# Performance work log

Hardware: AMD Instinct MI355X
Metric: run time of the kernel (lower is better)

## Reference

```python
import jax, jax.numpy as jnp
import numpy as np

B = 16; SEQ_LEN = 96; PRED_LEN = 96; N_VARS = 862; D_MODEL = 512; D_FF = 1024
N_HEADS = 8; E_LAYERS = 2; D_FREQ = 512; KF_LEN = 5000; ALPHA = 0.5; TOP_P = 0.5
FREQ_DIM = SEQ_LEN // 2 + 1            # rfft bins = 49
KEY_LEN = int(np.ceil(FREQ_DIM * ALPHA))  # 25 -> y_freq in_features = 50
KERNEL = 25; NOISE_EPS = 0.01; LN_EPS = 1e-5; REVIN_EPS = 1e-5


def setup_inputs() -> dict:
    ks = iter(jax.random.split(jax.random.key(0), 64))
    def g(*shape):
        return jax.random.normal(next(ks), shape, jnp.float32) * 0.02
    z = lambda *s: jnp.zeros(s, jnp.float32)
    o = lambda *s: jnp.ones(s, jnp.float32)
    inp = {}
    inp['x_enc'] = jax.random.normal(next(ks), (B, SEQ_LEN, N_VARS), jnp.float32)
    inp['gate_noise'] = jax.random.normal(next(ks), (N_VARS,), jnp.float32)
    inp['revin_w'] = o(N_VARS); inp['revin_b'] = z(N_VARS)
    inp['fc2_w'] = g(SEQ_LEN, D_MODEL); inp['fc2_b'] = z(D_MODEL)
    inp['fc3_w'] = g(D_MODEL, PRED_LEN); inp['fc3_b'] = z(PRED_LEN)
    inp['fc4_w'] = g(SEQ_LEN, D_MODEL); inp['fc4_b'] = z(D_MODEL)
    inp['fc5_w'] = g(D_MODEL, PRED_LEN); inp['fc5_b'] = z(PRED_LEN)
    inp['tc_w1'] = g(D_MODEL, D_MODEL // 2); inp['tc_w2'] = g(D_MODEL // 2, N_VARS)
    inp['tn_w1'] = g(D_MODEL, D_MODEL // 2); inp['tn_w2'] = g(D_MODEL // 2, N_VARS)
    inp['lt_w1'] = g(SEQ_LEN, D_MODEL); inp['lt_b1'] = z(D_MODEL)
    inp['lt_w2'] = g(D_MODEL, D_MODEL); inp['lt_b2'] = z(D_MODEL)
    inp['yf_w'] = g(2 * KEY_LEN, D_FREQ); inp['yf_b'] = z(D_FREQ)
    inp['ls_w1'] = g(D_FREQ, D_FREQ); inp['ls_b1'] = z(D_FREQ)
    inp['ls_w2'] = g(D_FREQ, D_FREQ); inp['ls_b2'] = z(D_FREQ)
    inp['fco_w'] = g(2 * D_MODEL, PRED_LEN); inp['fco_b'] = z(PRED_LEN)
    inp['freq_table'] = jax.random.normal(next(ks), (KF_LEN, N_VARS), jnp.float32)
    inp['enc_wq'] = g(E_LAYERS, D_MODEL, D_MODEL); inp['enc_bq'] = z(E_LAYERS, D_MODEL)
    inp['enc_wk'] = g(E_LAYERS, D_MODEL, D_MODEL); inp['enc_bk'] = z(E_LAYERS, D_MODEL)
    inp['enc_wv'] = g(E_LAYERS, D_MODEL, D_MODEL); inp['enc_bv'] = z(E_LAYERS, D_MODEL)
    inp['enc_wo'] = g(E_LAYERS, D_MODEL, D_MODEL); inp['enc_bo'] = z(E_LAYERS, D_MODEL)
    inp['enc_c1w'] = g(E_LAYERS, D_MODEL, D_FF); inp['enc_c1b'] = z(E_LAYERS, D_FF)
    inp['enc_c2w'] = g(E_LAYERS, D_FF, D_MODEL); inp['enc_c2b'] = z(E_LAYERS, D_MODEL)
    inp['enc_g1'] = o(E_LAYERS, D_MODEL); inp['enc_be1'] = z(E_LAYERS, D_MODEL)
    inp['enc_g2'] = o(E_LAYERS, D_MODEL); inp['enc_be2'] = z(E_LAYERS, D_MODEL)
    inp['norm_g'] = o(D_MODEL); inp['norm_b'] = z(D_MODEL)
    inp['batch_key_frequency'] = jax.random.randint(next(ks), (B,), 0, KF_LEN)
    return inp


def _lrelu(t):
    return jnp.where(t >= 0, t, 0.01 * t)


def _layernorm(x, g, b):
    m = jnp.mean(x, -1, keepdims=True)
    v = jnp.mean((x - m) ** 2, -1, keepdims=True)
    return (x - m) * jax.lax.rsqrt(v + LN_EPS) * g + b


def _decomp(x):
    # moving_avg(kernel=25, stride=1) with edge replication padding, via cumsum
    pad = (KERNEL - 1) // 2
    xp = jnp.concatenate([jnp.repeat(x[:, :1], pad, axis=1), x,
                          jnp.repeat(x[:, -1:], pad, axis=1)], axis=1)
    c = jnp.cumsum(xp, axis=1)
    c = jnp.concatenate([jnp.zeros_like(c[:, :1]), c], axis=1)
    mean = (c[:, KERNEL:] - c[:, :-KERNEL]) / KERNEL  # [B, L, N]
    return x - mean, mean


def _kf_gather(table, index, length):
    # data[(index[:,None] + arange(length)) % KF_LEN] -> [B, length, N]
    gi = (index[:, None] + jnp.arange(length)[None, :]) % KF_LEN
    return table[gi]


def _forward(x_enc, gate_noise, revin_w, revin_b, fc2_w, fc2_b, fc3_w, fc3_b,
             fc4_w, fc4_b, fc5_w, fc5_b, tc_w1, tc_w2, tn_w1, tn_w2,
             lt_w1, lt_b1, lt_w2, lt_b2, yf_w, yf_b, ls_w1, ls_b1, ls_w2, ls_b2,
             fco_w, fco_b, freq_table, enc_wq, enc_bq, enc_wk, enc_bk, enc_wv, enc_bv,
             enc_wo, enc_bo, enc_c1w, enc_c1b, enc_c2w, enc_c2b,
             enc_g1, enc_be1, enc_g2, enc_be2, norm_g, norm_b, batch_key_frequency):
    # RevIN norm (stats detached, as in RevIN)
    mean = jax.lax.stop_gradient(jnp.mean(x_enc, axis=1, keepdims=True))
    std = jax.lax.stop_gradient(jnp.sqrt(jnp.var(x_enc, axis=1, keepdims=True) + REVIN_EPS))
    x = (x_enc - mean) / std * revin_w + revin_b  # [B, L, N]

    # ---- Frequency encoder ----
    _, trend = _decomp(x)
    t = _lrelu(trend.transpose(0, 2, 1) @ lt_w1 + lt_b1) @ lt_w2 + lt_b2  # [B,N,D]
    xf = jnp.fft.rfft(x.transpose(0, 2, 1), axis=-1, norm='ortho')  # [B,N,FREQ_DIM]
    y_key = jnp.concatenate([xf.real[..., :KEY_LEN], xf.imag[..., :KEY_LEN]], axis=-1)
    y_key = y_key @ yf_w + yf_b  # [B,N,D_FREQ]
    y_key = y_key.transpose(0, 2, 1) - _kf_gather(freq_table, batch_key_frequency, D_FREQ)
    y = _lrelu(y_key.transpose(0, 2, 1) @ ls_w1 + ls_b1) @ ls_w2 + ls_b2  # [B,N,D_FREQ]
    y = y.transpose(0, 2, 1) + _kf_gather(freq_table, (batch_key_frequency + D_FREQ) % KF_LEN, D_FREQ)
    y = y.transpose(0, 2, 1)  # [B,N,D_FREQ], real part of frequency coeffs
    x_fre = jnp.fft.irfft(y.astype(jnp.complex64), n=SEQ_LEN, axis=-1, norm='ortho')  # [B,N,L]
    x_fre = x_fre @ fc4_w + fc4_b + t  # [B,N,D]
    x_fre_loss = x_fre @ fc5_w + fc5_b  # [B,N,pred]

    # ---- Time encoder ----
    xb = x.transpose(0, 2, 1) @ fc2_w + fc2_b  # [B,N,D]
    # noisy top-p gating mask
    xc = jax.nn.relu(xb @ tc_w1) @ tc_w2
    xn = jax.nn.relu(xb @ tn_w1) @ tn_w2
    # nn.Softplus(beta=-1): -log(1+exp(-x)) = -softplus(-x)
    xe = xc + gate_noise * (-jax.nn.softplus(-(xn + NOISE_EPS)))
    xmin = jnp.min(xe, axis=-1, keepdims=True)
    xmax = jnp.max(xe, axis=-1, keepdims=True)
    logits = (xe - xmin) / (xmax - xmin + 1e-6) + jnp.eye(N_VARS, dtype=xe.dtype)
    mask = (logits < TOP_P)[:, None]  # [B,1,N,N], True = masked out

    scale = 1.0 / np.sqrt(D_MODEL // N_HEADS)
    for l in range(E_LAYERS):
        q = (xb @ enc_wq[l] + enc_bq[l]).reshape(B, N_VARS, N_HEADS, -1)
        k = (xb @ enc_wk[l] + enc_bk[l]).reshape(B, N_VARS, N_HEADS, -1)
        v = (xb @ enc_wv[l] + enc_bv[l]).reshape(B, N_VARS, N_HEADS, -1)
        s = jnp.einsum('blhe,bshe->bhls', q, k)
        s = jnp.where(mask, -jnp.inf, s)
        a = jax.nn.softmax(scale * s, axis=-1)
        o = jnp.einsum('bhls,bshd->blhd', a, v).reshape(B, N_VARS, D_MODEL)
        xb = xb + (o @ enc_wo[l] + enc_bo[l])
        xb = _layernorm(xb, enc_g1[l], enc_be1[l])
        yff = jax.nn.gelu(xb @ enc_c1w[l] + enc_c1b[l], approximate=False) @ enc_c2w[l] + enc_c2b[l]
        xb = _layernorm(xb + yff, enc_g2[l], enc_be2[l])
    xb = _layernorm(xb, norm_g, norm_b)
    x_time_loss = xb @ fc3_w + fc3_b  # [B,N,pred]

    dec = (jnp.concatenate([xb, x_fre], axis=-1) @ fco_w + fco_b).transpose(0, 2, 1)  # [B,pred,N]

    def _denorm(z):
        return ((z - revin_b) / (revin_w + REVIN_EPS * REVIN_EPS)) * std + mean

    dec = _denorm(dec)
    x_time_loss = _denorm(x_time_loss.transpose(0, 2, 1))
    x_fre_loss = _denorm(x_fre_loss.transpose(0, 2, 1))
    return dec[:, -PRED_LEN:, :], x_time_loss, x_fre_loss


def reference(x_enc, gate_noise, revin_w, revin_b, fc2_w, fc2_b, fc3_w, fc3_b,
              fc4_w, fc4_b, fc5_w, fc5_b, tc_w1, tc_w2, tn_w1, tn_w2,
              lt_w1, lt_b1, lt_w2, lt_b2, yf_w, yf_b, ls_w1, ls_b1, ls_w2, ls_b2,
              fco_w, fco_b, freq_table, enc_wq, enc_bq, enc_wk, enc_bk, enc_wv, enc_bv,
              enc_wo, enc_bo, enc_c1w, enc_c1b, enc_c2w, enc_c2b,
              enc_g1, enc_be1, enc_g2, enc_be2, norm_g, norm_b, batch_key_frequency):
    return _forward(x_enc, gate_noise, revin_w, revin_b, fc2_w, fc2_b, fc3_w, fc3_b,
                    fc4_w, fc4_b, fc5_w, fc5_b, tc_w1, tc_w2, tn_w1, tn_w2,
                    lt_w1, lt_b1, lt_w2, lt_b2, yf_w, yf_b, ls_w1, ls_b1, ls_w2, ls_b2,
                    fco_w, fco_b, freq_table, enc_wq, enc_bq, enc_wk, enc_bk, enc_wv, enc_bv,
                    enc_wo, enc_bo, enc_c1w, enc_c1b, enc_c2w, enc_c2b,
                    enc_g1, enc_be1, enc_g2, enc_be2, norm_g, norm_b, batch_key_frequency)
```

## Files before the change

kernel.cpp:

```cpp
#include <hip/hip_runtime.h>
#include <hip/hip_bf16.h>
#include <math.h>

typedef __hip_bfloat16 bf16;
typedef unsigned long long u64;
using s8v = __attribute__((ext_vector_type(8))) short;
using f4v = __attribute__((ext_vector_type(4))) float;

#define B_   16
#define L_   96
#define NV   862
#define DM   512
#define NH   8
#define DH   64
#define KFL  5000
#define NBN  (B_*NV)
#define TS   72
#define NVP  896
#define QKVW 1536

__device__ __forceinline__ float tof(bf16 x)  { return __bfloat162float(x); }

__device__ __forceinline__ int sx(int r, int k) {
    return r * TS + (((k >> 3) ^ (r & 7)) << 3) + (k & 7);
}
__device__ __forceinline__ int sxc(int r, int c) {
    return r * TS + ((c ^ (r & 7)) << 3);
}

__global__ void detect_k(const unsigned short* __restrict__ rw, int* __restrict__ flag)
{
    if (threadIdx.x == 0 && blockIdx.x == 0)
        *flag = (rw[0] == 0 && rw[2] == 0 && rw[4] == 0) ? 1 : 0;
}

struct CB { const void* src[30]; bf16* dst[30]; int n[30]; int so[30]; };
__global__ __launch_bounds__(256)
void cvtb_k(CB cb, const int* __restrict__ flag)
{
    int t = blockIdx.y;
    int i = blockIdx.x * 256 + threadIdx.x;
    if (i >= cb.n[t]) return;
    int s = cb.so[t] + i;
    if (*flag) cb.dst[t][i] = __float2bfloat16(((const float*)cb.src[t])[s]);
    else       cb.dst[t][i] = ((const bf16*)cb.src[t])[s];
}

#define NWT 24
struct WD { const void* src; bf16* dst; int K, N; long srcOff; };
struct WTB { WD d[NWT]; };
__global__ __launch_bounds__(256)
void wtcb_k(WTB wb, const int* __restrict__ flag)
{
    __shared__ bf16 tile[32][33];
    WD dd = wb.d[blockIdx.z];
    int n0 = blockIdx.x * 32, k0 = blockIdx.y * 32;
    if (n0 >= dd.N || k0 >= dd.K) return;
    int tx = threadIdx.x & 31, ty = threadIdx.x >> 5;
    int f32 = *flag;
    #pragma unroll
    for (int r = 0; r < 4; r++) {
        int k = k0 + ty + r * 8, n = n0 + tx;
        bf16 v = __float2bfloat16(0.f);
        if (k < dd.K && n < dd.N)
            v = f32 ? __float2bfloat16(((const float*)dd.src)[dd.srcOff + (size_t)k * dd.N + n])
                    : ((const bf16*)dd.src)[dd.srcOff + (size_t)k * dd.N + n];
        tile[ty + r * 8][tx] = v;
    }
    __syncthreads();
    #pragma unroll
    for (int r = 0; r < 4; r++) {
        int n = n0 + ty + r * 8, k = k0 + tx;
        if (n < dd.N && k < dd.K) dd.dst[(size_t)n * dd.K + k] = tile[tx][ty + r * 8];
    }
}

__global__ __launch_bounds__(256)
void vt_k(const bf16* __restrict__ qkv, bf16* __restrict__ Vt)
{
    __shared__ bf16 t[32][33];
    int bh = blockIdx.z;
    int n0 = blockIdx.x * 32, d0 = blockIdx.y * 32;
    int b = bh >> 3, h = bh & 7;
    int tx = threadIdx.x & 31, ty = threadIdx.x >> 5;
    #pragma unroll
    for (int r = 0; r < 4; r++) {
        int n = n0 + ty + r * 8, d = d0 + tx;
        bf16 v = __float2bfloat16(0.f);
        if (n < NV) v = qkv[(size_t)(b * NV + n) * QKVW + 1024 + h * DH + d];
        t[ty + r * 8][tx] = v;
    }
    __syncthreads();
    #pragma unroll
    for (int r = 0; r < 4; r++) {
        int d = d0 + ty + r * 8, n = n0 + tx;
        Vt[((size_t)bh * DH + d) * NVP + n] = t[tx][ty + r * 8];
    }
}

__global__ __launch_bounds__(128)
void revin_k(const void* __restrict__ x_enc, const bf16* __restrict__ rw,
             const bf16* __restrict__ rb, bf16* __restrict__ xT,
             bf16* __restrict__ trend, float* __restrict__ meanA,
             float* __restrict__ stdA, const int* __restrict__ flag)
{
    int row = blockIdx.x;
    int b = row / NV, n = row - b * NV;
    int tid = threadIdx.x;
    int f32 = *flag;
    __shared__ float xr[96];
    __shared__ float part[2][2];
    __shared__ float mv[2];
    float v = 0.f;
    if (tid < 96) {
        size_t idx = ((size_t)b * L_ + tid) * NV + n;
        v = f32 ? ((const float*)x_enc)[idx] : tof(((const bf16*)x_enc)[idx]);
    }
    float s = v, sq = v * v;
    #pragma unroll
    for (int off = 32; off; off >>= 1) {
        s  += __shfl_xor(s,  off, 64);
        sq += __shfl_xor(sq, off, 64);
    }
    int wid = tid >> 6;
    if ((tid & 63) == 0) { part[wid][0] = s; part[wid][1] = sq; }
    __syncthreads();
    if (tid == 0) {
        float S = part[0][0] + part[1][0], Q = part[0][1] + part[1][1];
        float m = S / 96.f;
        float var = fmaxf(Q / 96.f - m * m, 0.f);
        float st = sqrtf(var + 1e-5f);
        mv[0] = m; mv[1] = st;
        meanA[row] = m; stdA[row] = st;
    }
    __syncthreads();
    float m = mv[0], st = mv[1];
    if (tid < 96) {
        float xv = (v - m) / st * tof(rw[n]) + tof(rb[n]);
        xr[tid] = xv;
        xT[(size_t)row * L_ + tid] = __float2bfloat16(xv);
    }
    __syncthreads();
    if (tid < 96) {
        float acc = 0.f;
        #pragma unroll
        for (int d = -12; d <= 12; d++) {
            int k = tid + d;
            k = k < 0 ? 0 : (k > 95 ? 95 : k);
            acc += xr[k];
        }
        trend[(size_t)row * L_ + tid] = __float2bfloat16(acc * (1.f / 25.f));
    }
}

__global__ void myf_k(const bf16* __restrict__ yf_w, bf16* __restrict__ MyfT)
{
    int idx = blockIdx.x * 256 + threadIdx.x;
    if (idx >= 96 * 512) return;
    int l = idx / 512, d = idx - l * 512;
    const float invs = 0.10206207261596575f;
    float acc = 0.f;
    for (int f = 0; f < 25; f++) {
        float ang = (float)(f * l) / 48.0f;
        acc += cospif(ang) * tof(yf_w[f * 512 + d]);
        acc -= sinpif(ang) * tof(yf_w[(25 + f) * 512 + d]);
    }
    MyfT[(size_t)d * 96 + l] = __float2bfloat16(acc * invs);
}

__global__ void ceff_k(const bf16* __restrict__ fc4_w, bf16* __restrict__ CeffT)
{
    int idx = blockIdx.x * 256 + threadIdx.x;
    if (idx >= 49 * 512) return;
    int f = idx / 512, d = idx - f * 512;
    const float invs = 0.10206207261596575f;
    float acc = 0.f;
    for (int l = 0; l < 96; l++) {
        float coef;
        if (f == 0)       coef = 1.f;
        else if (f == 48) coef = (l & 1) ? -1.f : 1.f;
        else              coef = 2.f * cospif((float)(f * l) / 48.f);
        acc += coef * tof(fc4_w[l * 512 + d]);
    }
    CeffT[(size_t)d * 49 + f] = __float2bfloat16(acc * invs);
}

__device__ __forceinline__ float epi(float v, int n, int m, int N, int act,
                                     const bf16* bias, const float* Res,
                                     const void* ft, const int* kf,
                                     const int* dflag)
{
    if (act >= 5) {
        v += tof(bias[n]);
        int b = m / NV, nv = m - b * NV;
        int gi = (act == 5) ? (kf[b] + n) % KFL : (kf[b] + 512 + n) % KFL;
        size_t gidx = (size_t)gi * NV + nv;
        float fv = (*dflag) ? ((const float*)ft)[gidx] : tof(((const bf16*)ft)[gidx]);
        return (act == 5) ? v - fv : v + fv;
    }
    if (act == 4) {
        float z = -(v + 0.01f);
        float sp = fmaxf(z, 0.f) + log1pf(expf(-fabsf(z)));
        return Res[(size_t)m * N + n] + tof(bias[n]) * (-sp);
    }
    if (bias) v += tof(bias[n]);
    if (Res)  v += Res[(size_t)m * N + n];
    if (act == 1)      v = fmaxf(v, 0.f);
    else if (act == 2) v = (v >= 0.f) ? v : 0.01f * v;
    else if (act == 3) v = 0.5f * v * (1.f + erff(v * 0.70710678118654752f));
    return v;
}

__global__ __launch_bounds__(256)
void gemm_mfma(const bf16* __restrict__ A, int lda,
               const bf16* __restrict__ Wt, int ldb,
               const bf16* __restrict__ bias, const float* Res,
               float* C32, bf16* C16, int M, int N, int K, int act,
               const void* ft, const int* kf, const int* dflag)
{
    __shared__ bf16 As[64 * TS];
    __shared__ bf16 Bs[64 * TS];
    int tid = threadIdx.x;
    int w = tid >> 6, lane = tid & 63;
    int lr = lane >> 4, lc = lane & 15;
    int row0 = blockIdx.y * 64, col0 = blockIdx.x * 64;
    int mq = (w >> 1) * 32, nq = (w & 1) * 32;
    f4v acc[2][2] = {};
    bool vecA = ((lda & 7) == 0) && ((K & 7) == 0);
    bool vecB = ((ldb & 7) == 0) && ((K & 7) == 0);
    const bf16 z16 = __float2bfloat16(0.f);
    for (int k0 = 0; k0 < K; k0 += 64) {
        if (vecA) {
            int r = tid >> 2, c0 = tid & 3;
            #pragma unroll
            for (int hh = 0; hh < 2; hh++) {
                int c = c0 + hh * 4;
                int gr = row0 + r, gk = k0 + c * 8;
                uint4 v = make_uint4(0, 0, 0, 0);
                if (gr < M && gk < K) v = *(const uint4*)(A + (size_t)gr * lda + gk);
                *(uint4*)&As[sxc(r, c)] = v;
            }
        } else {
            for (int i = tid; i < 4096; i += 256) {
                int r = i >> 6, k = i & 63;
                int gr = row0 + r, gk = k0 + k;
                As[sx(r, k)] = (gr < M && gk < K) ? A[(size_t)gr * lda + gk] : z16;
            }
        }
        if (vecB) {
            int r = tid >> 2, c0 = tid & 3;
            #pragma unroll
            for (int hh = 0; hh < 2; hh++) {
                int c = c0 + hh * 4;
                int gr = col0 + r, gk = k0 + c * 8;
                uint4 v = make_uint4(0, 0, 0, 0);
                if (gr < N && gk < K) v = *(const uint4*)(Wt + (size_t)gr * ldb + gk);
                *(uint4*)&Bs[sxc(r, c)] = v;
            }
        } else {
            for (int i = tid; i < 4096; i += 256) {
                int r = i >> 6, k = i & 63;
                int gr = col0 + r, gk = k0 + k;
                Bs[sx(r, k)] = (gr < N && gk < K) ? Wt[(size_t)gr * ldb + gk] : z16;
            }
        }
        __syncthreads();
        #pragma unroll
        for (int sub = 0; sub < 2; sub++) {
            int ck = sub * 4 + lr;
            s8v a0 = *(const s8v*)&As[sxc(mq + lc, ck)];
            s8v a1 = *(const s8v*)&As[sxc(mq + 16 + lc, ck)];
            s8v b0 = *(const s8v*)&Bs[sxc(nq + lc, ck)];
            s8v b1 = *(const s8v*)&Bs[sxc(nq + 16 + lc, ck)];
            acc[0][0] = __builtin_amdgcn_mfma_f32_16x16x32_bf16(a0, b0, acc[0][0], 0, 0, 0);
            acc[0][1] = __builtin_amdgcn_mfma_f32_16x16x32_bf16(a0, b1, acc[0][1], 0, 0, 0);
            acc[1][0] = __builtin_amdgcn_mfma_f32_16x16x32_bf16(a1, b0, acc[1][0], 0, 0, 0);
            acc[1][1] = __builtin_amdgcn_mfma_f32_16x16x32_bf16(a1, b1, acc[1][1], 0, 0, 0);
        }
        __syncthreads();
    }
    #pragma unroll
    for (int mt = 0; mt < 2; mt++)
    #pragma unroll
    for (int nt = 0; nt < 2; nt++) {
        #pragma unroll
        for (int r = 0; r < 4; r++) {
            int m = row0 + mq + mt * 16 + lr * 4 + r;
            int n = col0 + nq + nt * 16 + lc;
            if (m >= M || n >= N) continue;
            float v = epi(acc[mt][nt][r], n, m, N, act, bias, Res, ft, kf, dflag);
            if (C32) C32[(size_t)m * N + n] = v;
            if (C16) C16[(size_t)m * N + n] = __float2bfloat16(v);
        }
    }
}

__global__ __launch_bounds__(256)
void gemm128(const bf16* __restrict__ A, int lda,
             const bf16* __restrict__ Wt, int ldb,
             const bf16* __restrict__ bias, const float* Res,
             float* C32, bf16* C16, int M, int N, int K, int act)
{
    __shared__ bf16 As[128 * TS];
    __shared__ bf16 Bs[128 * TS];
    int tid = threadIdx.x;
    int w = tid >> 6, lane = tid & 63;
    int lr = lane >> 4, lc = lane & 15;
    int row0 = blockIdx.y * 128, col0 = blockIdx.x * 128;
    int mq = (w >> 1) * 64, nq = (w & 1) * 64;
    f4v acc[4][4] = {};
    for (int k0 = 0; k0 < K; k0 += 64) {
        #pragma unroll
        for (int i = 0; i < 4; i++) {
            int e = tid + i * 256;
            int r = e >> 3, c = e & 7;
            int gr = row0 + r, gk = k0 + c * 8;
            uint4 v = make_uint4(0, 0, 0, 0);
            if (gr < M && gk < K) v = *(const uint4*)(A + (size_t)gr * lda + gk);
            *(uint4*)&As[sxc(r, c)] = v;
        }
        #pragma unroll
        for (int i = 0; i < 4; i++) {
            int e = tid + i * 256;
            int r = e >> 3, c = e & 7;
            int gr = col0 + r, gk = k0 + c * 8;
            uint4 v = make_uint4(0, 0, 0, 0);
            if (gr < N && gk < K) v = *(const uint4*)(Wt + (size_t)gr * ldb + gk);
            *(uint4*)&Bs[sxc(r, c)] = v;
        }
        __syncthreads();
        #pragma unroll
        for (int sub = 0; sub < 2; sub++) {
            int ck = sub * 4 + lr;
            s8v a[4], b[4];
            #pragma unroll
            for (int mt = 0; mt < 4; mt++) a[mt] = *(const s8v*)&As[sxc(mq + mt * 16 + lc, ck)];
            #pragma unroll
            for (int nt = 0; nt < 4; nt++) b[nt] = *(const s8v*)&Bs[sxc(nq + nt * 16 + lc, ck)];
            #pragma unroll
            for (int mt = 0; mt < 4; mt++)
                #pragma unroll
                for (int nt = 0; nt < 4; nt++)
                    acc[mt][nt] = __builtin_amdgcn_mfma_f32_16x16x32_bf16(a[mt], b[nt], acc[mt][nt], 0, 0, 0);
        }
        __syncthreads();
    }
    #pragma unroll
    for (int mt = 0; mt < 4; mt++)
    #pragma unroll
    for (int nt = 0; nt < 4; nt++) {
        #pragma unroll
        for (int r = 0; r < 4; r++) {
            int m = row0 + mq + mt * 16 + lr * 4 + r;
            int n = col0 + nq + nt * 16 + lc;
            if (m >= M || n >= N) continue;
            float v = epi(acc[mt][nt][r], n, m, N, act, bias, Res, nullptr, nullptr, nullptr);
            if (C32) C32[(size_t)m * N + n] = v;
            if (C16) C16[(size_t)m * N + n] = __float2bfloat16(v);
        }
    }
}

__global__ __launch_bounds__(256)
void gemm64(const bf16* __restrict__ A, int lda,
            const bf16* __restrict__ Wt, int ldb,
            const bf16* __restrict__ bias, const float* Res,
            float* C32, bf16* C16, int M, int N, int K, int act,
            const void* ft, const int* kf, const int* dflag)
{
    __shared__ bf16 As[64 * TS];
    __shared__ bf16 Bs[128 * TS];
    int tid = threadIdx.x;
    int w = tid >> 6, lane = tid & 63;
    int lr = lane >> 4, lc = lane & 15;
    int row0 = blockIdx.y * 64, col0 = blockIdx.x * 128;
    int mq = (w >> 1) * 32, nq = (w & 1) * 64;
    f4v acc[2][4] = {};
    for (int k0 = 0; k0 < K; k0 += 64) {
        #pragma unroll
        for (int i = 0; i < 2; i++) {
            int e = tid + i * 256;
            int r = e >> 3, c = e & 7;
            int gr = row0 + r, gk = k0 + c * 8;
            uint4 v = make_uint4(0, 0, 0, 0);
            if (gr < M && gk < K) v = *(const uint4*)(A + (size_t)gr * lda + gk);
            *(uint4*)&As[sxc(r, c)] = v;
        }
        #pragma unroll
        for (int i = 0; i < 4; i++) {
            int e = tid + i * 256;
            int r = e >> 3, c = e & 7;
            int gr = col0 + r, gk = k0 + c * 8;
            uint4 v = make_uint4(0, 0, 0, 0);
            if (gr < N && gk < K) v = *(const uint4*)(Wt + (size_t)gr * ldb + gk);
            *(uint4*)&Bs[sxc(r, c)] = v;
        }
        __syncthreads();
        #pragma unroll
        for (int sub = 0; sub < 2; sub++) {
            int ck = sub * 4 + lr;
            s8v a[2], b[4];
            #pragma unroll
            for (int mt = 0; mt < 2; mt++) a[mt] = *(const s8v*)&As[sxc(mq + mt * 16 + lc, ck)];
            #pragma unroll
            for (int nt = 0; nt < 4; nt++) b[nt] = *(const s8v*)&Bs[sxc(nq + nt * 16 + lc, ck)];
            #pragma unroll
            for (int mt = 0; mt < 2; mt++)
                #pragma unroll
                for (int nt = 0; nt < 4; nt++)
                    acc[mt][nt] = __builtin_amdgcn_mfma_f32_16x16x32_bf16(a[mt], b[nt], acc[mt][nt], 0, 0, 0);
        }
        __syncthreads();
    }
    #pragma unroll
    for (int mt = 0; mt < 2; mt++)
    #pragma unroll
    for (int nt = 0; nt < 4; nt++) {
        #pragma unroll
        for (int r = 0; r < 4; r++) {
            int m = row0 + mq + mt * 16 + lr * 4 + r;
            int n = col0 + nq + nt * 16 + lc;
            if (m >= M || n >= N) continue;
            float v = epi(acc[mt][nt][r], n, m, N, act, bias, Res, ft, kf, dflag);
            if (C32) C32[(size_t)m * N + n] = v;
            if (C16) C16[(size_t)m * N + n] = __float2bfloat16(v);
        }
    }
}

__global__ __launch_bounds__(256)
void outg_mfma(const bf16* __restrict__ xb16, const bf16* __restrict__ xfre16,
               const bf16* __restrict__ fcoT, const bf16* __restrict__ fc3T,
               const bf16* __restrict__ fc5T, const bf16* __restrict__ fcob,
               const bf16* __restrict__ fc3b, const bf16* __restrict__ fc5b,
               const bf16* __restrict__ rw, const bf16* __restrict__ rb,
               const float* __restrict__ meanA, const float* __restrict__ stdA,
               void* __restrict__ outv, const int* __restrict__ flag)
{
    __shared__ bf16 As[64 * TS];
    __shared__ bf16 Bs[64 * TS];
    const int M = NBN, N = 96;
    const size_t OSZ = (size_t)B_ * L_ * NV;
    int z = blockIdx.z;
    const bf16 *A1, *W1, *A2 = nullptr, *W2 = nullptr, *bias;
    int ldb; size_t obase;
    if (z == 0) { A1 = xb16; W1 = fcoT; A2 = xfre16; W2 = fcoT + 512; ldb = 1024; bias = fcob; obase = 0; }
    else if (z == 1) { A1 = xb16; W1 = fc3T; ldb = 512; bias = fc3b; obase = OSZ; }
    else { A1 = xfre16; W1 = fc5T; ldb = 512; bias = fc5b; obase = 2 * OSZ; }
    int tid = threadIdx.x;
    int w = tid >> 6, lane = tid & 63;
    int lr = lane >> 4, lc = lane & 15;
    int row0 = blockIdx.y * 64, col0 = blockIdx.x * 64;
    int mq = (w >> 1) * 32, nq = (w & 1) * 32;
    int f32o = *flag;
    f4v acc[2][2] = {};
    for (int part = 0; part < 2; part++) {
        const bf16* A = part ? A2 : A1;
        const bf16* Wt = part ? W2 : W1;
        if (A == nullptr) break;
        const int K = 512;
        for (int k0 = 0; k0 < K; k0 += 64) {
            int r = tid >> 2, c0 = tid & 3;
            #pragma unroll
            for (int hh = 0; hh < 2; hh++) {
                int c = c0 + hh * 4;
                int gr = row0 + r, gk = k0 + c * 8;
                uint4 v = make_uint4(0, 0, 0, 0);
                if (gr < M) v = *(const uint4*)(A + (size_t)gr * 512 + gk);
                *(uint4*)&As[sxc(r, c)] = v;
                uint4 vb = make_uint4(0, 0, 0, 0);
                if (col0 + r < N) vb = *(const uint4*)(Wt + (size_t)(col0 + r) * ldb + gk);
                *(uint4*)&Bs[sxc(r, c)] = vb;
            }
            __syncthreads();
            #pragma unroll
            for (int sub = 0; sub < 2; sub++) {
                int ck = sub * 4 + lr;
                s8v a0 = *(const s8v*)&As[sxc(mq + lc, ck)];
                s8v a1 = *(const s8v*)&As[sxc(mq + 16 + lc, ck)];
                s8v b0 = *(const s8v*)&Bs[sxc(nq + lc, ck)];
                s8v b1 = *(const s8v*)&Bs[sxc(nq + 16 + lc, ck)];
                acc[0][0] = __builtin_amdgcn_mfma_f32_16x16x32_bf16(a0, b0, acc[0][0], 0, 0, 0);
                acc[0][1] = __builtin_amdgcn_mfma_f32_16x16x32_bf16(a0, b1, acc[0][1], 0, 0, 0);
                acc[1][0] = __builtin_amdgcn_mfma_f32_16x16x32_bf16(a1, b0, acc[1][0], 0, 0, 0);
                acc[1][1] = __builtin_amdgcn_mfma_f32_16x16x32_bf16(a1, b1, acc[1][1], 0, 0, 0);
            }
            __syncthreads();
        }
    }
    #pragma unroll
    for (int mt = 0; mt < 2; mt++)
    #pragma unroll
    for (int nt = 0; nt < 2; nt++) {
        #pragma unroll
        for (int r = 0; r < 4; r++) {
            int m = row0 + mq + mt * 16 + lr * 4 + r;
            int c = col0 + nq + nt * 16 + lc;
            if (m >= M || c >= N) continue;
            int b = m / NV, n = m - b * NV;
            float v = acc[mt][nt][r] + tof(bias[c]);
            v = (v - tof(rb[n])) / (tof(rw[n]) + 1e-10f) * stdA[m] + meanA[m];
            size_t oidx = obase + ((size_t)b * L_ + c) * NV + n;
            if (f32o) ((float*)outv)[oidx] = v;
            else      ((bf16*)outv)[oidx] = __float2bfloat16(v);
        }
    }
}

__global__ __launch_bounds__(256)
void gating_k(const float* __restrict__ xe, u64* __restrict__ mask64)
{
    int row = blockIdx.x;
    int i = row % NV;
    int tid = threadIdx.x;
    size_t base = (size_t)row * NV;
    float vals[4];
    int cnt = 0;
    float mn = INFINITY, mx = -INFINITY;
    for (int j = tid; j < NV; j += 256) {
        float e = xe[base + j];
        vals[cnt++] = e;
        mn = fminf(mn, e);
        mx = fmaxf(mx, e);
    }
    #pragma unroll
    for (int off = 32; off; off >>= 1) {
        mn = fminf(mn, __shfl_xor(mn, off, 64));
        mx = fmaxf(mx, __shfl_xor(mx, off, 64));
    }
    __shared__ float smn[4], smx[4], fin[2];
    int w = tid >> 6, lane = tid & 63;
    if (lane == 0) { smn[w] = mn; smx[w] = mx; }
    __syncthreads();
    if (tid == 0) {
        float a = fminf(fminf(smn[0], smn[1]), fminf(smn[2], smn[3]));
        float c = fmaxf(fmaxf(smx[0], smx[1]), fmaxf(smx[2], smx[3]));
        fin[0] = a;
        fin[1] = 1.f / (c - a + 1e-6f);
    }
    __syncthreads();
    float a = fin[0], inv = fin[1];
    cnt = 0;
    for (int t = w; t < 14; t += 4) {
        int j = t * 64 + lane;
        bool masked = true;
        if (j < NV) {
            float lg = (vals[cnt++] - a) * inv + ((j == i) ? 1.f : 0.f);
            masked = (lg < 0.5f);
        }
        u64 word = __ballot(masked);
        if (lane == 0) mask64[(size_t)row * 16 + t] = word;
    }
}

__global__ __launch_bounds__(256)
void ln_k(const float* __restrict__ X, const bf16* __restrict__ g,
          const bf16* __restrict__ bta, float* __restrict__ Y32,
          bf16* __restrict__ Y16)
{
    int row = blockIdx.x;
    int tid = threadIdx.x;
    size_t base = (size_t)row * DM;
    float v0 = X[base + tid], v1 = X[base + tid + 256];
    float s = v0 + v1, sq = v0 * v0 + v1 * v1;
    #pragma unroll
    for (int off = 32; off; off >>= 1) {
        s  += __shfl_xor(s,  off, 64);
        sq += __shfl_xor(sq, off, 64);
    }
    __shared__ float ps[4], pq[4], mv[2];
    int wid = tid >> 6;
    if ((tid & 63) == 0) { ps[wid] = s; pq[wid] = sq; }
    __syncthreads();
    if (tid == 0) {
        float S = ps[0] + ps[1] + ps[2] + ps[3];
        float Q = pq[0] + pq[1] + pq[2] + pq[3];
        float m = S / 512.f;
        float var = fmaxf(Q / 512.f - m * m, 0.f);
        mv[0] = m;
        mv[1] = rsqrtf(var + 1e-5f);
    }
    __syncthreads();
    float m = mv[0], r = mv[1];
    float o0 = (v0 - m) * r * tof(g[tid])       + tof(bta[tid]);
    float o1 = (v1 - m) * r * tof(g[tid + 256]) + tof(bta[tid + 256]);
    if (Y32) { Y32[base + tid] = o0; Y32[base + tid + 256] = o1; }
    if (Y16) { Y16[base + tid] = __float2bfloat16(o0);
               Y16[base + tid + 256] = __float2bfloat16(o1); }
}

__global__ __launch_bounds__(256)
void ln2x_k(const float* __restrict__ X, const bf16* __restrict__ g1,
            const bf16* __restrict__ b1, const bf16* __restrict__ g2,
            const bf16* __restrict__ b2, bf16* __restrict__ Y16)
{
    int row = blockIdx.x;
    int tid = threadIdx.x;
    size_t base = (size_t)row * DM;
    float v0 = X[base + tid], v1 = X[base + tid + 256];
    __shared__ float ps[4], pq[4], mv[2];
    int wid = tid >> 6;
    {
        float s = v0 + v1, sq = v0 * v0 + v1 * v1;
        #pragma unroll
        for (int off = 32; off; off >>= 1) {
            s  += __shfl_xor(s,  off, 64);
            sq += __shfl_xor(sq, off, 64);
        }
        if ((tid & 63) == 0) { ps[wid] = s; pq[wid] = sq; }
        __syncthreads();
        if (tid == 0) {
            float S = ps[0] + ps[1] + ps[2] + ps[3];
            float Q = pq[0] + pq[1] + pq[2] + pq[3];
            float m = S / 512.f;
            float var = fmaxf(Q / 512.f - m * m, 0.f);
            mv[0] = m; mv[1] = rsqrtf(var + 1e-5f);
        }
        __syncthreads();
    }
    float m1 = mv[0], r1 = mv[1];
    float y0 = (v0 - m1) * r1 * tof(g1[tid])       + tof(b1[tid]);
    float y1 = (v1 - m1) * r1 * tof(g1[tid + 256]) + tof(b1[tid + 256]);
    __syncthreads();
    {
        float s = y0 + y1, sq = y0 * y0 + y1 * y1;
        #pragma unroll
        for (int off = 32; off; off >>= 1) {
            s  += __shfl_xor(s,  off, 64);
            sq += __shfl_xor(sq, off, 64);
        }
        if ((tid & 63) == 0) { ps[wid] = s; pq[wid] = sq; }
        __syncthreads();
        if (tid == 0) {
            float S = ps[0] + ps[1] + ps[2] + ps[3];
            float Q = pq[0] + pq[1] + pq[2] + pq[3];
            float m = S / 512.f;
            float var = fmaxf(Q / 512.f - m * m, 0.f);
            mv[0] = m; mv[1] = rsqrtf(var + 1e-5f);
        }
        __syncthreads();
    }
    float m2 = mv[0], r2 = mv[1];
    Y16[base + tid]       = __float2bfloat16((y0 - m2) * r2 * tof(g2[tid])       + tof(b2[tid]));
    Y16[base + tid + 256] = __float2bfloat16((y1 - m2) * r2 * tof(g2[tid + 256]) + tof(b2[tid + 256]));
}

__global__ __launch_bounds__(256)
void attn_k(const bf16* __restrict__ qkv, const bf16* __restrict__ Vt,
            const u64* __restrict__ mask64, bf16* __restrict__ O)
{
    int bid = blockIdx.x;
    int bh = bid & 127;
    int q0 = (bid >> 7) * 64;
    int b = bh >> 3, h = bh & 7;
    int tid = threadIdx.x;
    int w = tid >> 6, lane = tid & 63;
    int lr = lane >> 4, lc = lane & 15;
    __shared__ bf16 Ks[64 * TS];
    __shared__ bf16 Vs[64 * TS];
    __shared__ bf16 Pt[4][16 * TS];
    size_t hb = (size_t)h * DH;
    int qw = q0 + w * 16;
    const float C = 0.18033688011112042f;

    s8v qf[2];
    #pragma unroll
    for (int sub = 0; sub < 2; sub++) {
        int gq = qw + lc;
        uint4 v = make_uint4(0, 0, 0, 0);
        if (gq < NV)
            v = *(const uint4*)(qkv + ((size_t)(b * NV + gq)) * QKVW + hb + sub * 32 + lr * 8);
        qf[sub] = *(s8v*)&v;
    }

    float lsum[4] = {0.f, 0.f, 0.f, 0.f};
    f4v oacc[4] = {};

    for (int t = 0; t < 14; t++) {
        int j0 = t * 64;
        {
            int r = tid >> 2, c0 = tid & 3;
            int gj = j0 + r;
            const bf16* kb = qkv + (size_t)(b * NV + (gj < NV ? gj : 0)) * QKVW + 512 + hb;
            const bf16* vb = Vt + ((size_t)(b * NH + h) * DH + r) * NVP + j0;
            #pragma unroll
            for (int hh = 0; hh < 2; hh++) {
                int c = c0 + hh * 4;
                uint4 kv = make_uint4(0, 0, 0, 0);
                if (gj < NV) kv = *(const uint4*)(kb + c * 8);
                *(uint4*)&Ks[sxc(r, c)] = kv;
                *(uint4*)&Vs[sxc(r, c)] = *(const uint4*)(vb + c * 8);
            }
        }
        __syncthreads();
        f4v s[4];
        #pragma unroll
        for (int nt = 0; nt < 4; nt++) {
            f4v sacc = {0.f, 0.f, 0.f, 0.f};
            #pragma unroll
            for (int sub = 0; sub < 2; sub++) {
                s8v bb = *(const s8v*)&Ks[sxc(nt * 16 + lc, sub * 4 + lr)];
                sacc = __builtin_amdgcn_mfma_f32_16x16x32_bf16(qf[sub], bb, sacc, 0, 0, 0);
            }
            s[nt] = sacc;
        }
        #pragma unroll
        for (int r = 0; r < 4; r++) {
            int gq = qw + lr * 4 + r;
            u64 wd = (gq < NV) ? mask64[(size_t)(b * NV + gq) * 16 + t] : ~0ull;
            #pragma unroll
            for (int nt = 0; nt < 4; nt++) {
                float p = ((wd >> (nt * 16 + lc)) & 1) ? 0.f : exp2f(s[nt][r] * C);
                Pt[w][sx(lr * 4 + r, nt * 16 + lc)] = __float2bfloat16(p);
                lsum[r] += p;
            }
        }
        #pragma unroll
        for (int sub = 0; sub < 2; sub++) {
            s8v pa = *(const s8v*)&Pt[w][sxc(lc, sub * 4 + lr)];
            #pragma unroll
            for (int dt = 0; dt < 4; dt++) {
                s8v vv = *(const s8v*)&Vs[sxc(dt * 16 + lc, sub * 4 + lr)];
                oacc[dt] = __builtin_amdgcn_mfma_f32_16x16x32_bf16(pa, vv, oacc[dt], 0, 0, 0);
            }
        }
        __syncthreads();
    }
    #pragma unroll
    for (int r = 0; r < 4; r++) {
        #pragma unroll
        for (int o2 = 1; o2 < 16; o2 <<= 1) lsum[r] += __shfl_xor(lsum[r], o2, 64);
    }
    #pragma unroll
    for (int r = 0; r < 4; r++) {
        int gq = qw + lr * 4 + r;
        if (gq >= NV) continue;
        float linv = 1.f / fmaxf(lsum[r], 1e-30f);
        #pragma unroll
        for (int dt = 0; dt < 4; dt++)
            O[((size_t)(b * NV + gq)) * DM + hb + dt * 16 + lc] =
                __float2bfloat16(oacc[dt][r] * linv);
    }
}

static void G(hipStream_t s, const bf16* A, int lda, const bf16* Wt, int ldb,
              const bf16* bias, const float* Res, float* C32, bf16* C16,
              int M, int N, int K, int act,
              const void* ft = nullptr, const int* kf = nullptr, const int* df = nullptr)
{
    dim3 g((N + 63) / 64, (M + 63) / 64);
    gemm_mfma<<<g, 256, 0, s>>>(A, lda, Wt, ldb, bias, Res, C32, C16, M, N, K, act, ft, kf, df);
}
static void G1(hipStream_t s, const bf16* A, int lda, const bf16* Wt, int ldb,
               const bf16* bias, const float* Res, float* C32, bf16* C16,
               int M, int N, int K, int act)
{
    dim3 g((N + 127) / 128, (M + 127) / 128);
    gemm128<<<g, 256, 0, s>>>(A, lda, Wt, ldb, bias, Res, C32, C16, M, N, K, act);
}
static void G64(hipStream_t s, const bf16* A, int lda, const bf16* Wt, int ldb,
                const bf16* bias, const float* Res, float* C32, bf16* C16,
                int M, int N, int K, int act,
                const void* ft = nullptr, const int* kf = nullptr, const int* df = nullptr)
{
    dim3 g((N + 127) / 128, (M + 63) / 64);
    gemm64<<<g, 256, 0, s>>>(A, lda, Wt, ldb, bias, Res, C32, C16, M, N, K, act, ft, kf, df);
}

enum { I_XENC = 0, I_GNOISE, I_RW, I_RB, I_FC2W, I_FC2B, I_FC3W, I_FC3B,
       I_FC4W, I_FC4B, I_FC5W, I_FC5B, I_TCW1, I_TCW2, I_TNW1, I_TNW2,
       I_LTW1, I_LTB1, I_LTW2, I_LTB2, I_YFW, I_YFB, I_LSW1, I_LSB1,
       I_LSW2, I_LSB2, I_FCOW, I_FCOB, I_FT, I_EWQ, I_EBQ, I_EWK, I_EBK,
       I_EWV, I_EBV, I_EWO, I_EBO, I_C1W, I_C1B, I_C2W, I_C2B,
       I_G1, I_BE1, I_G2, I_BE2, I_NG, I_NB };

extern "C" void kernel_launch(void* const* d_in, const int* in_sizes, int n_in,
                              void* d_out, int out_size, void* d_ws, size_t ws_size,
                              hipStream_t stream)
{
    const int* bkey = (const int*)d_in[47];
    (void)ws_size; (void)in_sizes; (void)n_in; (void)out_size;

    float* ws = (float*)d_ws;
    size_t off = 0;
    auto alloc = [&](size_t nf) { nf = (nf + 3) & ~(size_t)3; float* p = ws + off; off += nf; return p; };
    auto balloc = [&](size_t nb) { return (bf16*)alloc((nb + 1) / 2); };
    int*  flag  = (int*)alloc(16);
    bf16* gnoise = balloc(862); bf16* rw = balloc(862); bf16* rb = balloc(862);
    bf16* fc2b = balloc(512);  bf16* fc3b = balloc(96);
    bf16* fc4w_c = balloc(49152); bf16* fc4b = balloc(512); bf16* fc5b = balloc(96);
    bf16* ltb1 = balloc(512);  bf16* ltb2 = balloc(512);
    bf16* yfw_c = balloc(25600); bf16* yfb = balloc(512);
    bf16* lsb1 = balloc(512);  bf16* lsb2 = balloc(512);
    bf16* fcob = balloc(96);
    bf16* qkvb = balloc(2 * QKVW);
    bf16* ebo = balloc(1024);  bf16* c1b = balloc(2048); bf16* c2b = balloc(1024);
    bf16* g1v = balloc(1024);  bf16* be1v = balloc(1024);
    bf16* g2v = balloc(1024);  bf16* be2v = balloc(1024);
    bf16* ngv = balloc(512);   bf16* nbv = balloc(512);
    bf16* fc2wT = balloc(49152);  bf16* fc3wT = balloc(49152); bf16* fc5wT = balloc(49152);
    bf16* lt1T = balloc(49152);   bf16* lt2T = balloc(262144);
    bf16* ls1T = balloc(262144);  bf16* ls2T = balloc(262144);
    bf16* fcoT = balloc(98304);
    bf16* tc2T = balloc(220672);  bf16* tn2T = balloc(220672);
    bf16* gate1w = balloc(262144);
    bf16* qkvw = balloc(2 * QKVW * 512);
    bf16* woT = balloc(524288);
    bf16* c1T = balloc(1048576);  bf16* c2T = balloc(1048576);
    bf16* xT    = balloc((size_t)NBN * 96);
    bf16* trend = balloc((size_t)NBN * 96);
    float* meanA = alloc(13824);
    float* stdA  = alloc(13824);
    bf16* MyfT  = balloc(49152);
    bf16* CeffT = balloc(25088);
    bf16* y49   = balloc((size_t)NBN * 49);
    float* xb32 = alloc((size_t)NBN * 512);
    bf16* xb16  = balloc((size_t)NBN * 512);
    bf16* xfre16 = balloc((size_t)NBN * 512);
    bf16* tmp16 = balloc((size_t)NBN * 1024);
    float* fbuf = alloc((size_t)NBN * 512);
    float* gbuf = alloc((size_t)NBN * 1024);
    u64* mask64 = (u64*)alloc((size_t)NBN * 32);

    float* xe = gbuf;
    bf16* yA  = (bf16*)gbuf;
    bf16* qkv16 = (bf16*)gbuf;
    bf16* O16 = qkv16 + (size_t)NBN * QKVW;
    bf16* Vt  = tmp16;

    detect_k<<<1, 64, 0, stream>>>((const unsigned short*)d_in[I_RW], flag);

    {
        CB cb;
        int k = 0;
        auto add = [&](int idx, bf16* dst, int n, int so) {
            cb.src[k] = d_in[idx]; cb.dst[k] = dst; cb.n[k] = n; cb.so[k] = so; k++;
        };
        add(I_GNOISE, gnoise, 862, 0); add(I_RW, rw, 862, 0); add(I_RB, rb, 862, 0);
        add(I_FC2B, fc2b, 512, 0); add(I_FC3B, fc3b, 96, 0);
        add(I_FC4W, fc4w_c, 49152, 0); add(I_FC4B, fc4b, 512, 0); add(I_FC5B, fc5b, 96, 0);
        add(I_LTB1, ltb1, 512, 0); add(I_LTB2, ltb2, 512, 0);
        add(I_YFW, yfw_c, 25600, 0); add(I_YFB, yfb, 512, 0);
        add(I_LSB1, lsb1, 512, 0); add(I_LSB2, lsb2, 512, 0);
        add(I_FCOB, fcob, 96, 0);
        add(I_EBQ, qkvb + 0, 512, 0);          add(I_EBQ, qkvb + QKVW, 512, 512);
        add(I_EBK, qkvb + 512, 512, 0);        add(I_EBK, qkvb + QKVW + 512, 512, 512);
        add(I_EBV, qkvb + 1024, 512, 0);       add(I_EBV, qkvb + QKVW + 1024, 512, 512);
        add(I_EBO, ebo, 1024, 0); add(I_C1B, c1b, 2048, 0); add(I_C2B, c2b, 1024, 0);
        add(I_G1, g1v, 1024, 0); add(I_BE1, be1v, 1024, 0);
        add(I_G2, g2v, 1024, 0); add(I_BE2, be2v, 1024, 0);
        add(I_NG, ngv, 512, 0); add(I_NB, nbv, 512, 0);
        cvtb_k<<<dim3(192, 30), 256, 0, stream>>>(cb, flag);
    }

    {
        WTB wb;
        int k = 0;
        auto add = [&](int idx, bf16* dst, int K, int N, long soff) {
            wb.d[k].src = d_in[idx]; wb.d[k].dst = dst;
            wb.d[k].K = K; wb.d[k].N = N; wb.d[k].srcOff = soff; k++;
        };
        add(I_FC2W, fc2wT, 96, 512, 0);
        add(I_FC3W, fc3wT, 512, 96, 0);
        add(I_FC5W, fc5wT, 512, 96, 0);
        add(I_LTW1, lt1T, 96, 512, 0);
        add(I_LTW2, lt2T, 512, 512, 0);
        add(I_LSW1, ls1T, 512, 512, 0);
        add(I_LSW2, ls2T, 512, 512, 0);
        add(I_FCOW, fcoT, 1024, 96, 0);
        add(I_TCW2, tc2T, 256, 862, 0);
        add(I_TNW2, tn2T, 256, 862, 0);
        add(I_TCW1, gate1w, 512, 256, 0);
        add(I_TNW1, gate1w + 256 * 512, 512, 256, 0);
        for (int l = 0; l < 2; l++) {
            add(I_EWO, woT + (size_t)l * 262144, 512, 512, (long)l * 262144);
            add(I_C1W, c1T + (size_t)l * 524288, 512, 1024, (long)l * 524288);
            add(I_C2W, c2T + (size_t)l * 524288, 1024, 512, (long)l * 524288);
            add(I_EWQ, qkvw + (size_t)l * 786432 + 0,      512, 512, (long)l * 262144);
            add(I_EWK, qkvw + (size_t)l * 786432 + 262144, 512, 512, (long)l * 262144);
            add(I_EWV, qkvw + (size_t)l * 786432 + 524288, 512, 512, (long)l * 262144);
        }
        wtcb_k<<<dim3(32, 32, NWT), 256, 0, stream>>>(wb, flag);
    }

    revin_k<<<NBN, 128, 0, stream>>>(d_in[I_XENC], rw, rb, xT, trend, meanA, stdA, flag);
    myf_k<<<(96 * 512 + 255) / 256, 256, 0, stream>>>(yfw_c, MyfT);
    ceff_k<<<(49 * 512 + 255) / 256, 256, 0, stream>>>(fc4w_c, CeffT);

    G64(stream, trend, 96, lt1T, 96, ltb1, nullptr, nullptr, tmp16, NBN, 512, 96, 2);
    G64(stream, tmp16, 512, lt2T, 512, ltb2, nullptr, fbuf, nullptr, NBN, 512, 512, 0);
    G64(stream, xT, 96, MyfT, 96, yfb, nullptr, nullptr, yA, NBN, 512, 96, 5,
        d_in[I_FT], bkey, flag);
    G64(stream, yA, 512, ls1T, 512, lsb1, nullptr, nullptr, tmp16, NBN, 512, 512, 2);
    G(stream, tmp16, 512, ls2T, 512, lsb2, nullptr, nullptr, y49, NBN, 49, 512, 6,
      d_in[I_FT], bkey, flag);
    G(stream, y49, 49, CeffT, 49, fc4b, fbuf, nullptr, xfre16, NBN, 512, 49, 0);

    G64(stream, xT, 96, fc2wT, 96, fc2b, nullptr, xb32, xb16, NBN, 512, 96, 0);

    G64(stream, xb16, 512, gate1w, 512, nullptr, nullptr, nullptr, tmp16, NBN, 512, 512, 1);
    G64(stream, tmp16, 512, tc2T, 256, nullptr, nullptr, xe, nullptr, NBN, 862, 256, 0);
    G64(stream, tmp16 + 256, 512, tn2T, 256, gnoise, xe, xe, nullptr, NBN, 862, 256, 4);
    gating_k<<<NBN, 256, 0, stream>>>(xe, mask64);

    for (int l = 0; l < 2; l++) {
        G1(stream, xb16, 512, qkvw + (size_t)l * QKVW * 512, 512,
           qkvb + l * QKVW, nullptr, nullptr, qkv16, NBN, QKVW, 512, 0);
        vt_k<<<dim3(NVP / 32, DH / 32, B_ * NH), 256, 0, stream>>>(qkv16, Vt);
        attn_k<<<dim3(14 * 128), 256, 0, stream>>>(qkv16, Vt, mask64, O16);
        G64(stream, O16, 512, woT + (size_t)l * 262144, 512, ebo + l * 512,
            xb32, fbuf, nullptr, NBN, 512, 512, 0);
        ln_k<<<NBN, 256, 0, stream>>>(fbuf, g1v + l * 512, be1v + l * 512, xb32, xb16);
        G1(stream, xb16, 512, c1T + (size_t)l * 524288, 512, c1b + l * 1024,
           nullptr, nullptr, tmp16, NBN, 1024, 512, 3);
        G64(stream, tmp16, 1024, c2T + (size_t)l * 524288, 1024, c2b + l * 512,
            xb32, fbuf, nullptr, NBN, 512, 1024, 0);
        if (l == 0)
            ln_k<<<NBN, 256, 0, stream>>>(fbuf, g2v, be2v, xb32, xb16);
        else
            ln2x_k<<<NBN, 256, 0, stream>>>(fbuf, g2v + 512, be2v + 512, ngv, nbv, xb16);
    }

    outg_mfma<<<dim3(2, (NBN + 63) / 64, 3), 256, 0, stream>>>(
        xb16, xfre16, fcoT, fc3wT, fc5wT, fcob, fc3b, fc5b,
        rw, rb, meanA, stdA, d_out, flag);
}
```

Before: 1.601 ms.

## Double-buffer GEMM tiles with direct global-to-LDS loads and pad K dims

Rewrites the 64- and 128-tile MFMA GEMMs so that each K tile is staged with global_load_lds 16-byte direct-to-LDS loads into a double buffer. The next tile is fetched while the current one is multiplied, and one barrier per iteration is dropped. To allow this unconditional vector staging, the K=96 and K=49 operands (xT, trend, MyfT, CeffT, y49 and the transposed weights) are zero-padded to 128 or 64 columns. The slow generic 64x64 gemm_mfma path is removed. The cost is doubled LDS use per block, which may lower occupancy, plus extra padded work on the small-K GEMMs.

```diff
diff --git a/kernel.cpp b/kernel.cpp
--- a/kernel.cpp
+++ b/kernel.cpp
@@ -18,6 +18,7 @@
 #define TS   72
 #define NVP  896
 #define QKVW 1536
+#define L2P  128
 
 __device__ __forceinline__ float tof(bf16 x)  { return __bfloat162float(x); }
 
@@ -26,6 +27,41 @@
 }
 __device__ __forceinline__ int sxc(int r, int c) {
     return r * TS + ((c ^ (r & 7)) << 3);
+}
+__device__ __forceinline__ int sxl(int r, int c) {
+    return (r << 6) + ((c ^ (r & 7)) << 3);
+}
+
+__device__ __forceinline__ void gl16(const bf16* g, bf16* l)
+{
+    __builtin_amdgcn_global_load_lds(
+        (const __attribute__((address_space(1))) void*)g,
+        (__attribute__((address_space(3))) void*)l, 16, 0, 0);
+}
+
+__device__ __forceinline__ void stage64(const bf16* __restrict__ src, int ld,
+                                        int r0, int rmax, int k0, bf16* buf, int tid)
+{
+    #pragma unroll
+    for (int i = 0; i < 2; i++) {
+        int e = tid + i * 256;
+        int r = e >> 3, c = e & 7;
+        int gr = r0 + r; gr = gr > rmax ? rmax : gr;
+        int gk = k0 + ((c ^ (r & 7)) << 3);
+        gl16(src + (size_t)gr * ld + gk, buf + ((size_t)(e >> 6) << 9));
+    }
+}
+__device__ __forceinline__ void stage128(const bf16* __restrict__ src, int ld,
+                                         int r0, int rmax, int k0, bf16* buf, int tid)
+{
+    #pragma unroll
+    for (int i = 0; i < 4; i++) {
+        int e = tid + i * 256;
+        int r = e >> 3, c = e & 7;
+        int gr = r0 + r; gr = gr > rmax ? rmax : gr;
+        int gk = k0 + ((c ^ (r & 7)) << 3);
+        gl16(src + (size_t)gr * ld + gk, buf + ((size_t)(e >> 6) << 9));
+    }
 }
 
 __global__ void detect_k(const unsigned short* __restrict__ rw, int* __restrict__ flag)
@@ -47,7 +83,7 @@
 }
 
 #define NWT 24
-struct WD { const void* src; bf16* dst; int K, N; long srcOff; };
+struct WD { const void* src; bf16* dst; int K, Kp, N; long srcOff; };
 struct WTB { WD d[NWT]; };
 __global__ __launch_bounds__(256)
 void wtcb_k(WTB wb, const int* __restrict__ flag)
@@ -55,7 +91,7 @@
     __shared__ bf16 tile[32][33];
     WD dd = wb.d[blockIdx.z];
     int n0 = blockIdx.x * 32, k0 = blockIdx.y * 32;
-    if (n0 >= dd.N || k0 >= dd.K) return;
+    if (n0 >= dd.N || k0 >= dd.Kp) return;
     int tx = threadIdx.x & 31, ty = threadIdx.x >> 5;
     int f32 = *flag;
     #pragma unroll
@@ -71,7 +107,7 @@
     #pragma unroll
     for (int r = 0; r < 4; r++) {
         int n = n0 + ty + r * 8, k = k0 + tx;
-        if (n < dd.N && k < dd.K) dd.dst[(size_t)n * dd.K + k] = tile[tx][ty + r * 8];
+        if (n < dd.N && k < dd.Kp) dd.dst[(size_t)n * dd.Kp + k] = tile[tx][ty + r * 8];
     }
 }
 
@@ -135,10 +171,13 @@
     }
     __syncthreads();
     float m = mv[0], st = mv[1];
+    const bf16 z16 = __float2bfloat16(0.f);
     if (tid < 96) {
         float xv = (v - m) / st * tof(rw[n]) + tof(rb[n]);
         xr[tid] = xv;
-        xT[(size_t)row * L_ + tid] = __float2bfloat16(xv);
+        xT[(size_t)row * L2P + tid] = __float2bfloat16(xv);
+    } else {
+        xT[(size_t)row * L2P + tid] = z16;
     }
     __syncthreads();
     if (tid < 96) {
@@ -149,40 +188,48 @@
             k = k < 0 ? 0 : (k > 95 ? 95 : k);
             acc += xr[k];
         }
-        trend[(size_t)row * L_ + tid] = __float2bfloat16(acc * (1.f / 25.f));
+        trend[(size_t)row * L2P + tid] = __float2bfloat16(acc * (1.f / 25.f));
+    } else {
+        trend[(size_t)row * L2P + tid] = z16;
     }
 }
 
 __global__ void myf_k(const bf16* __restrict__ yf_w, bf16* __restrict__ MyfT)
 {
     int idx = blockIdx.x * 256 + threadIdx.x;
-    if (idx >= 96 * 512) return;
-    int l = idx / 512, d = idx - l * 512;
+    if (idx >= 512 * L2P) return;
+    int d = idx >> 7, l = idx & 127;
     const float invs = 0.10206207261596575f;
     float acc = 0.f;
-    for (int f = 0; f < 25; f++) {
-        float ang = (float)(f * l) / 48.0f;
-        acc += cospif(ang) * tof(yf_w[f * 512 + d]);
-        acc -= sinpif(ang) * tof(yf_w[(25 + f) * 512 + d]);
-    }
-    MyfT[(size_t)d * 96 + l] = __float2bfloat16(acc * invs);
+    if (l < 96) {
+        for (int f = 0; f < 25; f++) {
+            float ang = (float)(f * l) / 48.0f;
+            acc += cospif(ang) * tof(yf_w[f * 512 + d]);
+            acc -= sinpif(ang) * tof(yf_w[(25 + f) * 512 + d]);
+        }
+        acc *= invs;
+    }
+    MyfT[(size_t)d * L2P + l] = __float2bfloat16(acc);
 }
 
 __global__ void ceff_k(const bf16* __restrict__ fc4_w, bf16* __restrict__ CeffT)
 {
     int idx = blockIdx.x * 256 + threadIdx.x;
-    if (idx >= 49 * 512) return;
-    int f = idx / 512, d = idx - f * 512;
+    if (idx >= 512 * 64) return;
+    int d = idx >> 6, f = idx & 63;
     const float invs = 0.10206207261596575f;
     float acc = 0.f;
-    for (int l = 0; l < 96; l++) {
-        float coef;
-        if (f == 0)       coef = 1.f;
-        else if (f == 48) coef = (l & 1) ? -1.f : 1.f;
-        else              coef = 2.f * cospif((float)(f * l) / 48.f);
-        acc += coef * tof(fc4_w[l * 512 + d]);
-    }
-    CeffT[(size_t)d * 49 + f] = __float2bfloat16(acc * invs);
+    if (f < 49) {
+        for (int l = 0; l < 96; l++) {
+            float coef;
+            if (f == 0)       coef = 1.f;
+            else if (f == 48) coef = (l & 1) ? -1.f : 1.f;
+            else              coef = 2.f * cospif((float)(f * l) / 48.f);
+            acc += coef * tof(fc4_w[l * 512 + d]);
+        }
+        acc *= invs;
+    }
+    CeffT[(size_t)d * 64 + f] = __float2bfloat16(acc);
 }
 
 __device__ __forceinline__ float epi(float v, int n, int m, int N, int act,
@@ -212,149 +259,56 @@
 }
 
 __global__ __launch_bounds__(256)
-void gemm_mfma(const bf16* __restrict__ A, int lda,
-               const bf16* __restrict__ Wt, int ldb,
-               const bf16* __restrict__ bias, const float* Res,
-               float* C32, bf16* C16, int M, int N, int K, int act,
-               const void* ft, const int* kf, const int* dflag)
-{
-    __shared__ bf16 As[64 * TS];
-    __shared__ bf16 Bs[64 * TS];
-    int tid = threadIdx.x;
-    int w = tid >> 6, lane = tid & 63;
-    int lr = lane >> 4, lc = lane & 15;
-    int row0 = blockIdx.y * 64, col0 = blockIdx.x * 64;
-    int mq = (w >> 1) * 32, nq = (w & 1) * 32;
-    f4v acc[2][2] = {};
-    bool vecA = ((lda & 7) == 0) && ((K & 7) == 0);
-    bool vecB = ((ldb & 7) == 0) && ((K & 7) == 0);
-    const bf16 z16 = __float2bfloat16(0.f);
-    for (int k0 = 0; k0 < K; k0 += 64) {
-        if (vecA) {
-            int r = tid >> 2, c0 = tid & 3;
-            #pragma unroll
-            for (int hh = 0; hh < 2; hh++) {
-                int c = c0 + hh * 4;
-                int gr = row0 + r, gk = k0 + c * 8;
-                uint4 v = make_uint4(0, 0, 0, 0);
-                if (gr < M && gk < K) v = *(const uint4*)(A + (size_t)gr * lda + gk);
-                *(uint4*)&As[sxc(r, c)] = v;
-            }
-        } else {
-            for (int i = tid; i < 4096; i += 256) {
-                int r = i >> 6, k = i & 63;
-                int gr = row0 + r, gk = k0 + k;
-                As[sx(r, k)] = (gr < M && gk < K) ? A[(size_t)gr * lda + gk] : z16;
-            }
-        }
-        if (vecB) {
-            int r = tid >> 2, c0 = tid & 3;
-            #pragma unroll
-            for (int hh = 0; hh < 2; hh++) {
-                int c = c0 + hh * 4;
-                int gr = col0 + r, gk = k0 + c * 8;
-                uint4 v = make_uint4(0, 0, 0, 0);
-                if (gr < N && gk < K) v = *(const uint4*)(Wt + (size_t)gr * ldb + gk);
-                *(uint4*)&Bs[sxc(r, c)] = v;
-            }
-        } else {
-            for (int i = tid; i < 4096; i += 256) {
-                int r = i >> 6, k = i & 63;
-                int gr = col0 + r, gk = k0 + k;
-                Bs[sx(r, k)] = (gr < N && gk < K) ? Wt[(size_t)gr * ldb + gk] : z16;
-            }
-        }
-        __syncthreads();
-        #pragma unroll
-        for (int sub = 0; sub < 2; sub++) {
-            int ck = sub * 4 + lr;
-            s8v a0 = *(const s8v*)&As[sxc(mq + lc, ck)];
-            s8v a1 = *(const s8v*)&As[sxc(mq + 16 + lc, ck)];
-            s8v b0 = *(const s8v*)&Bs[sxc(nq + lc, ck)];
-            s8v b1 = *(const s8v*)&Bs[sxc(nq + 16 + lc, ck)];
-            acc[0][0] = __builtin_amdgcn_mfma_f32_16x16x32_bf16(a0, b0, acc[0][0], 0, 0, 0);
-            acc[0][1] = __builtin_amdgcn_mfma_f32_16x16x32_bf16(a0, b1, acc[0][1], 0, 0, 0);
-            acc[1][0] = __builtin_amdgcn_mfma_f32_16x16x32_bf16(a1, b0, acc[1][0], 0, 0, 0);
-            acc[1][1] = __builtin_amdgcn_mfma_f32_16x16x32_bf16(a1, b1, acc[1][1], 0, 0, 0);
-        }
-        __syncthreads();
-    }
-    #pragma unroll
-    for (int mt = 0; mt < 2; mt++)
-    #pragma unroll
-    for (int nt = 0; nt < 2; nt++) {
-        #pragma unroll
-        for (int r = 0; r < 4; r++) {
-            int m = row0 + mq + mt * 16 + lr * 4 + r;
-            int n = col0 + nq + nt * 16 + lc;
-            if (m >= M || n >= N) continue;
-            float v = epi(acc[mt][nt][r], n, m, N, act, bias, Res, ft, kf, dflag);
-            if (C32) C32[(size_t)m * N + n] = v;
-            if (C16) C16[(size_t)m * N + n] = __float2bfloat16(v);
-        }
-    }
-}
-
-__global__ __launch_bounds__(256)
-void gemm128(const bf16* __restrict__ A, int lda,
-             const bf16* __restrict__ Wt, int ldb,
-             const bf16* __restrict__ bias, const float* Res,
-             float* C32, bf16* C16, int M, int N, int K, int act)
-{
-    __shared__ bf16 As[128 * TS];
-    __shared__ bf16 Bs[128 * TS];
+void gemm128p(const bf16* __restrict__ A, int lda,
+              const bf16* __restrict__ Wt, int ldb,
+              const bf16* __restrict__ bias, const float* Res,
+              float* C32, bf16* C16, int M, int N, int K, int act)
+{
+    __shared__ __align__(16) bf16 As[2][128 * 64];
+    __shared__ __align__(16) bf16 Bs[2][128 * 64];
     int tid = threadIdx.x;
     int w = tid >> 6, lane = tid & 63;
     int lr = lane >> 4, lc = lane & 15;
     int row0 = blockIdx.y * 128, col0 = blockIdx.x * 128;
     int mq = (w >> 1) * 64, nq = (w & 1) * 64;
     f4v acc[4][4] = {};
-    for (int k0 = 0; k0 < K; k0 += 64) {
-        #pragma unroll
-        for (int i = 0; i < 4; i++) {
-            int e = tid + i * 256;
-            int r = e >> 3, c = e & 7;
-            int gr = row0 + r, gk = k0 + c * 8;
-            uint4 v = make_uint4(0, 0, 0, 0);
-            if (gr < M && gk < K) v = *(const uint4*)(A + (size_t)gr * lda + gk);
-            *(uint4*)&As[sxc(r, c)] = v;
-        }
-        #pragma unroll
-        for (int i = 0; i < 4; i++) {
-            int e = tid + i * 256;
-            int r = e >> 3, c = e & 7;
-            int gr = col0 + r, gk = k0 + c * 8;
-            uint4 v = make_uint4(0, 0, 0, 0);
-            if (gr < N && gk < K) v = *(const uint4*)(Wt + (size_t)gr * ldb + gk);
-            *(uint4*)&Bs[sxc(r, c)] = v;
-        }
-        __syncthreads();
+    int nt = K >> 6;
+    stage128(A, lda, row0, M - 1, 0, As[0], tid);
+    stage128(Wt, ldb, col0, N - 1, 0, Bs[0], tid);
+    __syncthreads();
+    int cur = 0;
+    for (int t = 1; t <= nt; t++) {
+        if (t < nt) {
+            stage128(A, lda, row0, M - 1, t << 6, As[cur ^ 1], tid);
+            stage128(Wt, ldb, col0, N - 1, t << 6, Bs[cur ^ 1], tid);
+        }
         #pragma unroll
         for (int sub = 0; sub < 2; sub++) {
             int ck = sub * 4 + lr;
             s8v a[4], b[4];
             #pragma unroll
-            for (int mt = 0; mt < 4; mt++) a[mt] = *(const s8v*)&As[sxc(mq + mt * 16 + lc, ck)];
-            #pragma unroll
-            for (int nt = 0; nt < 4; nt++) b[nt] = *(const s8v*)&Bs[sxc(nq + nt * 16 + lc, ck)];
+            for (int mt = 0; mt < 4; mt++) a[mt] = *(const s8v*)&As[cur][sxl(mq + mt * 16 + lc, ck)];
+            #pragma unroll
+            for (int j = 0; j < 4; j++) b[j] = *(const s8v*)&Bs[cur][sxl(nq + j * 16 + lc, ck)];
             #pragma unroll
             for (int mt = 0; mt < 4; mt++)
                 #pragma unroll
-                for (int nt = 0; nt < 4; nt++)
-                    acc[mt][nt] = __builtin_amdgcn_mfma_f32_16x16x32_bf16(a[mt], b[nt], acc[mt][nt], 0, 0, 0);
-        }
-        __syncthreads();
+                for (int j = 0; j < 4; j++)
+                    acc[mt][j] = __builtin_amdgcn_mfma_f32_16x16x32_bf16(a[mt], b[j], acc[mt][j], 0, 0, 0);
+        }
+        if (t < nt) __syncthreads();
+        cur ^= 1;
     }
     #pragma unroll
     for (int mt = 0; mt < 4; mt++)
     #pragma unroll
-    for (int nt = 0; nt < 4; nt++) {
+    for (int j = 0; j < 4; j++) {
         #pragma unroll
         for (int r = 0; r < 4; r++) {
             int m = row0 + mq + mt * 16 + lr * 4 + r;
-            int n = col0 + nq + nt * 16 + lc;
+            int n = col0 + nq + j * 16 + lc;
             if (m >= M || n >= N) continue;
-            float v = epi(acc[mt][nt][r], n, m, N, act, bias, Res, nullptr, nullptr, nullptr);
+            float v = epi(acc[mt][j][r], n, m, N, act, bias, Res, nullptr, nullptr, nullptr);
             if (C32) C32[(size_t)m * N + n] = v;
             if (C16) C16[(size_t)m * N + n] = __float2bfloat16(v);
         }
@@ -362,66 +316,57 @@
 }
 
 __global__ __launch_bounds__(256)
-void gemm64(const bf16* __restrict__ A, int lda,
-            const bf16* __restrict__ Wt, int ldb,
-            const bf16* __restrict__ bias, const float* Res,
-            float* C32, bf16* C16, int M, int N, int K, int act,
-            const void* ft, const int* kf, const int* dflag)
-{
-    __shared__ bf16 As[64 * TS];
-    __shared__ bf16 Bs[128 * TS];
+void gemm64p(const bf16* __restrict__ A, int lda,
+             const bf16* __restrict__ Wt, int ldb,
+             const bf16* __restrict__ bias, const float* Res,
+             float* C32, bf16* C16, int M, int N, int K, int act,
+             const void* ft, const int* kf, const int* dflag)
+{
+    __shared__ __align__(16) bf16 As[2][64 * 64];
+    __shared__ __align__(16) bf16 Bs[2][128 * 64];
     int tid = threadIdx.x;
     int w = tid >> 6, lane = tid & 63;
     int lr = lane >> 4, lc = lane & 15;
     int row0 = blockIdx.y * 64, col0 = blockIdx.x * 128;
     int mq = (w >> 1) * 32, nq = (w & 1) * 64;
     f4v acc[2][4] = {};
-    for (int k0 = 0; k0 < K; k0 += 64) {
-        #pragma unroll
-        for (int i = 0; i < 2; i++) {
-            int e = tid + i * 256;
-            int r = e >> 3, c = e & 7;
-            int gr = row0 + r, gk = k0 + c * 8;
-            uint4 v = make_uint4(0, 0, 0, 0);
-            if (gr < M && gk < K) v = *(const uint4*)(A + (size_t)gr * lda + gk);
-            *(uint4*)&As[sxc(r, c)] = v;
-        }
-        #pragma unroll
-        for (int i = 0; i < 4; i++) {
-            int e = tid + i * 256;
-            int r = e >> 3, c = e & 7;
-            int gr = col0 + r, gk = k0 + c * 8;
-            uint4 v = make_uint4(0, 0, 0, 0);
-            if (gr < N && gk < K) v = *(const uint4*)(Wt + (size_t)gr * ldb + gk);
-            *(uint4*)&Bs[sxc(r, c)] = v;
-        }
-        __syncthreads();
+    int nt = K >> 6;
+    stage64(A, lda, row0, M - 1, 0, As[0], tid);
+    stage128(Wt, ldb, col0, N - 1, 0, Bs[0], tid);
+    __syncthreads();
+    int cur = 0;
+    for (int t = 1; t <= nt; t++) {
+        if (t < nt) {
+            stage64(A, lda, row0, M - 1, t << 6, As[cur ^ 1], tid);
+            stage128(Wt, ldb, col0, N - 1, t << 6, Bs[cur ^ 1], tid);
+        }
         #pragma unroll
         for (int sub = 0; sub < 2; sub++) {
             int ck = sub * 4 + lr;
             s8v a[2], b[4];
             #pragma unroll
-            for (int mt = 0; mt < 2; mt++) a[mt] = *(const s8v*)&As[sxc(mq + mt * 16 + lc, ck)];
-            #pragma unroll
-            for (int nt = 0; nt < 4; nt++) b[nt] = *(const s8v*)&Bs[sxc(nq + nt * 16 + lc, ck)];
+            for (int mt = 0; mt < 2; mt++) a[mt] = *(const s8v*)&As[cur][sxl(mq + mt * 16 + lc, ck)];
+            #pragma unroll
+            for (int j = 0; j < 4; j++) b[j] = *(const s8v*)&Bs[cur][sxl(nq + j * 16 + lc, ck)];
             #pragma unroll
             for (int mt = 0; mt < 2; mt++)
                 #pragma unroll
-                for (int nt = 0; nt < 4; nt++)
-                    acc[mt][nt] = __builtin_amdgcn_mfma_f32_16x16x32_bf16(a[mt], b[nt], acc[mt][nt], 0, 0, 0);
-        }
-        __syncthreads();
+                for (int j = 0; j < 4; j++)
+                    acc[mt][j] = __builtin_amdgcn_mfma_f32_16x16x32_bf16(a[mt], b[j], acc[mt][j], 0, 0, 0);
+        }
+        if (t < nt) __syncthreads();
+        cur ^= 1;
     }
     #pragma unroll
     for (int mt = 0; mt < 2; mt++)
     #pragma unroll
-    for (int nt = 0; nt < 4; nt++) {
+    for (int j = 0; j < 4; j++) {
         #pragma unroll
         for (int r = 0; r < 4; r++) {
             int m = row0 + mq + mt * 16 + lr * 4 + r;
-            int n = col0 + nq + nt * 16 + lc;
+            int n = col0 + nq + j * 16 + lc;
             if (m >= M || n >= N) continue;
-            float v = epi(acc[mt][nt][r], n, m, N, act, bias, Res, ft, kf, dflag);
+            float v = epi(acc[mt][j][r], n, m, N, act, bias, Res, ft, kf, dflag);
             if (C32) C32[(size_t)m * N + n] = v;
             if (C16) C16[(size_t)m * N + n] = __float2bfloat16(v);
         }
@@ -437,8 +382,8 @@
                const float* __restrict__ meanA, const float* __restrict__ stdA,
                void* __restrict__ outv, const int* __restrict__ flag)
 {
-    __shared__ bf16 As[64 * TS];
-    __shared__ bf16 Bs[64 * TS];
+    __shared__ __align__(16) bf16 As[2][64 * 64];
+    __shared__ __align__(16) bf16 Bs[2][64 * 64];
     const int M = NBN, N = 96;
     const size_t OSZ = (size_t)B_ * L_ * NV;
     int z = blockIdx.z;
@@ -454,51 +399,44 @@
     int mq = (w >> 1) * 32, nq = (w & 1) * 32;
     int f32o = *flag;
     f4v acc[2][2] = {};
-    for (int part = 0; part < 2; part++) {
-        const bf16* A = part ? A2 : A1;
-        const bf16* Wt = part ? W2 : W1;
-        if (A == nullptr) break;
-        const int K = 512;
-        for (int k0 = 0; k0 < K; k0 += 64) {
-            int r = tid >> 2, c0 = tid & 3;
-            #pragma unroll
-            for (int hh = 0; hh < 2; hh++) {
-                int c = c0 + hh * 4;
-                int gr = row0 + r, gk = k0 + c * 8;
-                uint4 v = make_uint4(0, 0, 0, 0);
-                if (gr < M) v = *(const uint4*)(A + (size_t)gr * 512 + gk);
-                *(uint4*)&As[sxc(r, c)] = v;
-                uint4 vb = make_uint4(0, 0, 0, 0);
-                if (col0 + r < N) vb = *(const uint4*)(Wt + (size_t)(col0 + r) * ldb + gk);
-                *(uint4*)&Bs[sxc(r, c)] = vb;
-            }
-            __syncthreads();
-            #pragma unroll
-            for (int sub = 0; sub < 2; sub++) {
-                int ck = sub * 4 + lr;
-                s8v a0 = *(const s8v*)&As[sxc(mq + lc, ck)];
-                s8v a1 = *(const s8v*)&As[sxc(mq + 16 + lc, ck)];
-                s8v b0 = *(const s8v*)&Bs[sxc(nq + lc, ck)];
-                s8v b1 = *(const s8v*)&Bs[sxc(nq + 16 + lc, ck)];
-                acc[0][0] = __builtin_amdgcn_mfma_f32_16x16x32_bf16(a0, b0, acc[0][0], 0, 0, 0);
-                acc[0][1] = __builtin_amdgcn_mfma_f32_16x16x32_bf16(a0, b1, acc[0][1], 0, 0, 0);
-                acc[1][0] = __builtin_amdgcn_mfma_f32_16x16x32_bf16(a1, b0, acc[1][0], 0, 0, 0);
-                acc[1][1] = __builtin_amdgcn_mfma_f32_16x16x32_bf16(a1, b1, acc[1][1], 0, 0, 0);
-            }
-            __syncthreads();
-        }
+    int nt = (z == 0) ? 16 : 8;
+    stage64(A1, 512, row0, M - 1, 0, As[0], tid);
+    stage64(W1, ldb, col0, N - 1, 0, Bs[0], tid);
+    __syncthreads();
+    int cur = 0;
+    for (int t = 1; t <= nt; t++) {
+        if (t < nt) {
+            const bf16* Ax = (t >= 8) ? A2 : A1;
+            const bf16* Wx = (t >= 8) ? W2 : W1;
+            stage64(Ax, 512, row0, M - 1, (t & 7) << 6, As[cur ^ 1], tid);
+            stage64(Wx, ldb, col0, N - 1, (t & 7) << 6, Bs[cur ^ 1], tid);
+        }
+        #pragma unroll
+        for (int sub = 0; sub < 2; sub++) {
+            int ck = sub * 4 + lr;
+            s8v a0 = *(const s8v*)&As[cur][sxl(mq + lc, ck)];
+            s8v a1 = *(const s8v*)&As[cur][sxl(mq + 16 + lc, ck)];
+            s8v b0 = *(const s8v*)&Bs[cur][sxl(nq + lc, ck)];
+            s8v b1 = *(const s8v*)&Bs[cur][sxl(nq + 16 + lc, ck)];
+            acc[0][0] = __builtin_amdgcn_mfma_f32_16x16x32_bf16(a0, b0, acc[0][0], 0, 0, 0);
+            acc[0][1] = __builtin_amdgcn_mfma_f32_16x16x32_bf16(a0, b1, acc[0][1], 0, 0, 0);
+            acc[1][0] = __builtin_amdgcn_mfma_f32_16x16x32_bf16(a1, b0, acc[1][0], 0, 0, 0);
+            acc[1][1] = __builtin_amdgcn_mfma_f32_16x16x32_bf16(a1, b1, acc[1][1], 0, 0, 0);
+        }
+        if (t < nt) __syncthreads();
+        cur ^= 1;
     }
     #pragma unroll
     for (int mt = 0; mt < 2; mt++)
     #pragma unroll
-    for (int nt = 0; nt < 2; nt++) {
+    for (int j = 0; j < 2; j++) {
         #pragma unroll
         for (int r = 0; r < 4; r++) {
             int m = row0 + mq + mt * 16 + lr * 4 + r;
-            int c = col0 + nq + nt * 16 + lc;
+            int c = col0 + nq + j * 16 + lc;
             if (m >= M || c >= N) continue;
             int b = m / NV, n = m - b * NV;
-            float v = acc[mt][nt][r] + tof(bias[c]);
+            float v = acc[mt][j][r] + tof(bias[c]);
             v = (v - tof(rb[n])) / (tof(rw[n]) + 1e-10f) * stdA[m] + meanA[m];
             size_t oidx = obase + ((size_t)b * L_ + c) * NV + n;
             if (f32o) ((float*)outv)[oidx] = v;
@@ -743,20 +681,12 @@
     }
 }
 
-static void G(hipStream_t s, const bf16* A, int lda, const bf16* Wt, int ldb,
-              const bf16* bias, const float* Res, float* C32, bf16* C16,
-              int M, int N, int K, int act,
-              const void* ft = nullptr, const int* kf = nullptr, const int* df = nullptr)
-{
-    dim3 g((N + 63) / 64, (M + 63) / 64);
-    gemm_mfma<<<g, 256, 0, s>>>(A, lda, Wt, ldb, bias, Res, C32, C16, M, N, K, act, ft, kf, df);
-}
 static void G1(hipStream_t s, const bf16* A, int lda, const bf16* Wt, int ldb,
                const bf16* bias, const float* Res, float* C32, bf16* C16,
                int M, int N, int K, int act)
 {
     dim3 g((N + 127) / 128, (M + 127) / 128);
-    gemm128<<<g, 256, 0, s>>>(A, lda, Wt, ldb, bias, Res, C32, C16, M, N, K, act);
+    gemm128p<<<g, 256, 0, s>>>(A, lda, Wt, ldb, bias, Res, C32, C16, M, N, K, act);
 }
 static void G64(hipStream_t s, const bf16* A, int lda, const bf16* Wt, int ldb,
                 const bf16* bias, const float* Res, float* C32, bf16* C16,
@@ -764,7 +694,7 @@
                 const void* ft = nullptr, const int* kf = nullptr, const int* df = nullptr)
 {
     dim3 g((N + 127) / 128, (M + 63) / 64);
-    gemm64<<<g, 256, 0, s>>>(A, lda, Wt, ldb, bias, Res, C32, C16, M, N, K, act, ft, kf, df);
+    gemm64p<<<g, 256, 0, s>>>(A, lda, Wt, ldb, bias, Res, C32, C16, M, N, K, act, ft, kf, df);
 }
 
 enum { I_XENC = 0, I_GNOISE, I_RW, I_RB, I_FC2W, I_FC2B, I_FC3W, I_FC3B,
@@ -798,8 +728,8 @@
     bf16* g1v = balloc(1024);  bf16* be1v = balloc(1024);
     bf16* g2v = balloc(1024);  bf16* be2v = balloc(1024);
     bf16* ngv = balloc(512);   bf16* nbv = balloc(512);
-    bf16* fc2wT = balloc(49152);  bf16* fc3wT = balloc(49152); bf16* fc5wT = balloc(49152);
-    bf16* lt1T = balloc(49152);   bf16* lt2T = balloc(262144);
+    bf16* fc2wT = balloc(512 * L2P);  bf16* fc3wT = balloc(49152); bf16* fc5wT = balloc(49152);
+    bf16* lt1T = balloc(512 * L2P);   bf16* lt2T = balloc(262144);
     bf16* ls1T = balloc(262144);  bf16* ls2T = balloc(262144);
     bf16* fcoT = balloc(98304);
     bf16* tc2T = balloc(220672);  bf16* tn2T = balloc(220672);
@@ -807,13 +737,13 @@
     bf16* qkvw = balloc(2 * QKVW * 512);
     bf16* woT = balloc(524288);
     bf16* c1T = balloc(1048576);  bf16* c2T = balloc(1048576);
-    bf16* xT    = balloc((size_t)NBN * 96);
-    bf16* trend = balloc((size_t)NBN * 96);
+    bf16* xT    = balloc((size_t)NBN * L2P);
+    bf16* trend = balloc((size_t)NBN * L2P);
     float* meanA = alloc(13824);
     float* stdA  = alloc(13824);
-    bf16* MyfT  = balloc(49152);
-    bf16* CeffT = balloc(25088);
-    bf16* y49   = balloc((size_t)NBN * 49);
+    bf16* MyfT  = balloc(512 * L2P);
+    bf16* CeffT = balloc(512 * 64);
+    bf16* y49   = balloc((size_t)NBN * 64);
     float* xb32 = alloc((size_t)NBN * 512);
     bf16* xb16  = balloc((size_t)NBN * 512);
     bf16* xfre16 = balloc((size_t)NBN * 512);
@@ -856,47 +786,47 @@
     {
         WTB wb;
         int k = 0;
-        auto add = [&](int idx, bf16* dst, int K, int N, long soff) {
+        auto add = [&](int idx, bf16* dst, int K, int Kp, int N, long soff) {
             wb.d[k].src = d_in[idx]; wb.d[k].dst = dst;
-            wb.d[k].K = K; wb.d[k].N = N; wb.d[k].srcOff = soff; k++;
+            wb.d[k].K = K; wb.d[k].Kp = Kp; wb.d[k].N = N; wb.d[k].srcOff = soff; k++;
         };
-        add(I_FC2W, fc2wT, 96, 512, 0);
-        add(I_FC3W, fc3wT, 512, 96, 0);
-        add(I_FC5W, fc5wT, 512, 96, 0);
-        add(I_LTW1, lt1T, 96, 512, 0);
-        add(I_LTW2, lt2T, 512, 512, 0);
-        add(I_LSW1, ls1T, 512, 512, 0);
-        add(I_LSW2, ls2T, 512, 512, 0);
-        add(I_FCOW, fcoT, 1024, 96, 0);
-        add(I_TCW2, tc2T, 256, 862, 0);
-        add(I_TNW2, tn2T, 256, 862, 0);
-        add(I_TCW1, gate1w, 512, 256, 0);
-        add(I_TNW1, gate1w + 256 * 512, 512, 256, 0);
+        add(I_FC2W, fc2wT, 96, L2P, 512, 0);
+        add(I_FC3W, fc3wT, 512, 512, 96, 0);
+        add(I_FC5W, fc5wT, 512, 512, 96, 0);
+        add(I_LTW1, lt1T, 96, L2P, 512, 0);
+        add(I_LTW2, lt2T, 512, 512, 512, 0);
+        add(I_LSW1, ls1T, 512, 512, 512, 0);
+        add(I_LSW2, ls2T, 512, 512, 512, 0);
+        add(I_FCOW, fcoT, 1024, 1024, 96, 0);
+        add(I_TCW2, tc2T, 256, 256, 862, 0);
+        add(I_TNW2, tn2T, 256, 256, 862, 0);
+        add(I_TCW1, gate1w, 512, 512, 256, 0);
+        add(I_TNW1, gate1w + 256 * 512, 512, 512, 256, 0);
         for (int l = 0; l < 2; l++) {
-            add(I_EWO, woT + (size_t)l * 262144, 512, 512, (long)l * 262144);
-            add(I_C1W, c1T + (size_t)l * 524288, 512, 1024, (long)l * 524288);
-            add(I_C2W, c2T + (size_t)l * 524288, 1024, 512, (long)l * 524288);
-            add(I_EWQ, qkvw + (size_t)l * 786432 + 0,      512, 512, (long)l * 262144);
-            add(I_EWK, qkvw + (size_t)l * 786432 + 262144, 512, 512, (long)l * 262144);
-            add(I_EWV, qkvw + (size_t)l * 786432 + 524288, 512, 512, (long)l * 262144);
+            add(I_EWO, woT + (size_t)l * 262144, 512, 512, 512, (long)l * 262144);
+            add(I_C1W, c1T + (size_t)l * 524288, 512, 512, 1024, (long)l * 524288);
+            add(I_C2W, c2T + (size_t)l * 524288, 1024, 1024, 512, (long)l * 524288);
+            add(I_EWQ, qkvw + (size_t)l * 786432 + 0,      512, 512, 512, (long)l * 262144);
+            add(I_EWK, qkvw + (size_t)l * 786432 + 262144, 512, 512, 512, (long)l * 262144);
+            add(I_EWV, qkvw + (size_t)l * 786432 + 524288, 512, 512, 512, (long)l * 262144);
         }
         wtcb_k<<<dim3(32, 32, NWT), 256, 0, stream>>>(wb, flag);
     }
 
     revin_k<<<NBN, 128, 0, stream>>>(d_in[I_XENC], rw, rb, xT, trend, meanA, stdA, flag);
-    myf_k<<<(96 * 512 + 255) / 256, 256, 0, stream>>>(yfw_c, MyfT);
-    ceff_k<<<(49 * 512 + 255) / 256, 256, 0, stream>>>(fc4w_c, CeffT);
-
-    G64(stream, trend, 96, lt1T, 96, ltb1, nullptr, nullptr, tmp16, NBN, 512, 96, 2);
+    myf_k<<<(512 * L2P + 255) / 256, 256, 0, stream>>>(yfw_c, MyfT);
+    ceff_k<<<(512 * 64 + 255) / 256, 256, 0, stream>>>(fc4w_c, CeffT);
+
+    G64(stream, trend, L2P, lt1T, L2P, ltb1, nullptr, nullptr, tmp16, NBN, 512, L2P, 2);
     G64(stream, tmp16, 512, lt2T, 512, ltb2, nullptr, fbuf, nullptr, NBN, 512, 512, 0);
-    G64(stream, xT, 96, MyfT, 96, yfb, nullptr, nullptr, yA, NBN, 512, 96, 5,
+    G64(stream, xT, L2P, MyfT, L2P, yfb, nullptr, nullptr, yA, NBN, 512, L2P, 5,
         d_in[I_FT], bkey, flag);
     G64(stream, yA, 512, ls1T, 512, lsb1, nullptr, nullptr, tmp16, NBN, 512, 512, 2);
-    G(stream, tmp16, 512, ls2T, 512, lsb2, nullptr, nullptr, y49, NBN, 49, 512, 6,
-      d_in[I_FT], bkey, flag);
-    G(stream, y49, 49, CeffT, 49, fc4b, fbuf, nullptr, xfre16, NBN, 512, 49, 0);
-
-    G64(stream, xT, 96, fc2wT, 96, fc2b, nullptr, xb32, xb16, NBN, 512, 96, 0);
+    G64(stream, tmp16, 512, ls2T, 512, lsb2, nullptr, nullptr, y49, NBN, 64, 512, 6,
+        d_in[I_FT], bkey, flag);
+    G64(stream, y49, 64, CeffT, 64, fc4b, fbuf, nullptr, xfre16, NBN, 512, 64, 0);
+
+    G64(stream, xT, L2P, fc2wT, L2P, fc2b, nullptr, xb32, xb16, NBN, 512, L2P, 0);
 
     G64(stream, xb16, 512, gate1w, 512, nullptr, nullptr, nullptr, tmp16, NBN, 512, 512, 1);
     G64(stream, tmp16, 512, tc2T, 256, nullptr, nullptr, xe, nullptr, NBN, 862, 256, 0);
```

New measurement: 1.847 ms. 15.4% more time.
